# Performance work log

Hardware: AMD Instinct MI355X
Metric: run time of the kernel (lower is better)

The kernel has to match this reference:

```python
import jax, jax.numpy as jnp
import numpy as np

B, C, INTER, T, H, W = 2, 256, 64, 8, 32, 32


def setup_inputs() -> dict:
    key = jax.random.key(0)
    ks = jax.random.split(key, 4)
    scale_q = 1.0 / np.sqrt(C)
    x = jax.random.normal(ks[0], (B, C, T, H, W), dtype=jnp.float32)
    Wq = jax.random.normal(ks[1], (INTER, C), dtype=jnp.float32) * scale_q
    Wk = jax.random.normal(ks[2], (INTER, C), dtype=jnp.float32) * scale_q
    Wv = jax.random.normal(ks[3], (C, C), dtype=jnp.float32) * scale_q
    return {
        "x": x,
        "Wq": Wq, "bq": jnp.zeros((INTER,), jnp.float32),
        "Wk": Wk, "bk": jnp.zeros((INTER,), jnp.float32),
        "Wv": Wv, "bv": jnp.zeros((C,), jnp.float32),
    }


def reference(x, Wq, bq, Wk, bk, Wv, bv):
    b, c, t, h, w = x.shape
    n = t * h * w
    xf = x.reshape(b, c, n)  # [B, C, N] (row-major flatten over T,H,W)
    # 1x1x1 Conv3d == per-voxel linear projection
    q = jnp.einsum('oc,bcn->bno', Wq, xf) + bq          # [B, N, INTER]
    k = jnp.einsum('oc,bcn->bon', Wk, xf) + bk[:, None]  # [B, INTER, N]
    v = jnp.einsum('oc,bcn->bon', Wv, xf) + bv[:, None]  # [B, C, N]
    energy = jnp.einsum('bid,bdj->bij', q, k)            # [B, N, N]
    attention = jax.nn.softmax(energy, axis=-1)
    # out[b,c,i] = sum_j v[b,c,j] * attention[b,i,j]
    out = jnp.einsum('bcj,bij->bci', v, attention)       # [B, C, N]
    out = out.reshape(b, c, t, h, w) + x
    return out
```

## Files before the change

### kernel.cpp

```cpp
#include <hip/hip_runtime.h>
#include <hip/hip_bf16.h>

typedef short short8 __attribute__((ext_vector_type(8)));
typedef float float4v __attribute__((ext_vector_type(4)));

#define MFMA(a, b, c) __builtin_amdgcn_mfma_f32_16x16x32_bf16((a), (b), (c), 0, 0, 0)

typedef const __attribute__((address_space(1))) unsigned int gu32;
typedef __attribute__((address_space(3))) unsigned int lu32;
#define GLOAD_LDS16(g, l) __builtin_amdgcn_global_load_lds((gu32*)(g), (lu32*)(l), 16, 0, 0)

#define LOG2E 1.4426950408889634f

static __device__ __forceinline__ unsigned short f2bf(float f) {
    union { float f; unsigned u; } v; v.f = f;
    unsigned r = (v.u + 0x7fffu + ((v.u >> 16) & 1u)) >> 16;
    return (unsigned short)r;
}
static __device__ __forceinline__ float bf2f(unsigned short h) {
    union { unsigned u; float f; } v; v.u = ((unsigned)h) << 16;
    return v.f;
}

static __device__ __forceinline__ int qk_idx(int b, int n, int o) {
    int frag = (b * 512 + (n >> 4)) * 2 + (o >> 5);
    return frag * 512 + ((o >> 3) & 3) * 128 + (n & 15) * 8 + (o & 7);
}
static __device__ __forceinline__ int v_idx(int b, int c, int n) {
    int frag = (b * 256 + (n >> 5)) * 16 + (c >> 4);
    return frag * 512 + ((n >> 3) & 3) * 128 + (c & 15) * 8 + (n & 7);
}

__global__ void wcvt(const float* __restrict__ Wq, const float* __restrict__ Wk,
                     const float* __restrict__ Wv,
                     unsigned short* __restrict__ Whi, unsigned short* __restrict__ Wlo) {
    int idx = blockIdx.x * 256 + threadIdx.x;
    if (idx >= 384 * 256) return;
    int row = idx >> 8, c = idx & 255;
    float f;
    if (row < 64)       f = Wq[row * 256 + c];
    else if (row < 128) f = Wk[(row - 64) * 256 + c];
    else                f = Wv[(row - 128) * 256 + c];
    unsigned short hi = f2bf(f);
    Whi[idx] = hi;
    if (row < 128) Wlo[idx] = f2bf(f - bf2f(hi));
}

__global__ __launch_bounds__(256, 1) void proj(
        const float* __restrict__ x, const unsigned short* __restrict__ Whi,
        const unsigned short* __restrict__ Wlo,
        const float* __restrict__ bq, const float* __restrict__ bk,
        const float* __restrict__ bv,
        unsigned short* __restrict__ qhi_ws, unsigned short* __restrict__ qlo_ws,
        unsigned short* __restrict__ khi_ws, unsigned short* __restrict__ klo_ws,
        unsigned short* __restrict__ vws) {
    __shared__ unsigned short XThi[64 * 264];
    __shared__ unsigned short XTlo[64 * 264];

    const int tid = threadIdx.x;
    const int b  = blockIdx.x >> 7;
    const int n0 = (blockIdx.x & 127) << 6;
    const float* xb = x + b * 2097152;

    for (int p = 0; p < 16; ++p) {
        int idx = p * 256 + tid;
        int c = idx >> 4, nq = idx & 15;
        float4v xv = *reinterpret_cast<const float4v*>(xb + c * 8192 + n0 + nq * 4);
#pragma unroll
        for (int q = 0; q < 4; ++q) {
            unsigned short hi = f2bf(xv[q]);
            XThi[(nq * 4 + q) * 264 + c] = hi;
            XTlo[(nq * 4 + q) * 264 + c] = f2bf(xv[q] - bf2f(hi));
        }
    }
    __syncthreads();

    const int lane = tid & 63, w = tid >> 6;
    const int quad = lane >> 4, l16 = lane & 15;

    short8 aXhi[8], aXlo[8];
#pragma unroll
    for (int ks = 0; ks < 8; ++ks) {
        aXhi[ks] = *reinterpret_cast<const short8*>(&XThi[(w * 16 + l16) * 264 + ks * 32 + quad * 8]);
        aXlo[ks] = *reinterpret_cast<const short8*>(&XTlo[(w * 16 + l16) * 264 + ks * 32 + quad * 8]);
    }

#pragma unroll
    for (int ot = 0; ot < 8; ++ot) {
        float4v acc = {0.f, 0.f, 0.f, 0.f};
#pragma unroll
        for (int ks = 0; ks < 8; ++ks) {
            short8 bwhi = *reinterpret_cast<const short8*>(&Whi[(ot * 16 + l16) * 256 + ks * 32 + quad * 8]);
            short8 bwlo = *reinterpret_cast<const short8*>(&Wlo[(ot * 16 + l16) * 256 + ks * 32 + quad * 8]);
            acc = MFMA(aXhi[ks], bwhi, acc);
            acc = MFMA(aXlo[ks], bwhi, acc);
            acc = MFMA(aXhi[ks], bwlo, acc);
        }
        int o = ot * 16 + l16;
        float bias = (ot < 4) ? bq[o] : bk[o - 64];
#pragma unroll
        for (int r = 0; r < 4; ++r) {
            int n = n0 + w * 16 + quad * 4 + r;
            float y = acc[r] + bias;
            if (ot < 4) y *= LOG2E;
            unsigned short hi = f2bf(y);
            unsigned short lo = f2bf(y - bf2f(hi));
            if (ot < 4) {
                int id = qk_idx(b, n, o);
                qhi_ws[id] = hi; qlo_ws[id] = lo;
            } else {
                int id = qk_idx(b, n, o - 64);
                khi_ws[id] = hi; klo_ws[id] = lo;
            }
        }
    }

    float4v acc2[4][4];
#pragma unroll
    for (int mt = 0; mt < 4; ++mt)
#pragma unroll
        for (int nt = 0; nt < 4; ++nt) acc2[mt][nt] = (float4v){0.f, 0.f, 0.f, 0.f};

#pragma unroll
    for (int ks = 0; ks < 8; ++ks) {
        short8 aW[4], bX[4];
#pragma unroll
        for (int mt = 0; mt < 4; ++mt)
            aW[mt] = *reinterpret_cast<const short8*>(&Whi[(128 + w * 64 + mt * 16 + l16) * 256 + ks * 32 + quad * 8]);
#pragma unroll
        for (int nt = 0; nt < 4; ++nt)
            bX[nt] = *reinterpret_cast<const short8*>(&XThi[(nt * 16 + l16) * 264 + ks * 32 + quad * 8]);
#pragma unroll
        for (int mt = 0; mt < 4; ++mt)
#pragma unroll
            for (int nt = 0; nt < 4; ++nt)
                acc2[mt][nt] = MFMA(aW[mt], bX[nt], acc2[mt][nt]);
    }
#pragma unroll
    for (int mt = 0; mt < 4; ++mt) {
#pragma unroll
        for (int r = 0; r < 4; ++r) {
            int c = w * 64 + mt * 16 + quad * 4 + r;
            float bias = bv[c];
#pragma unroll
            for (int nt = 0; nt < 4; ++nt) {
                int n = n0 + nt * 16 + l16;
                vws[v_idx(b, c, n)] = f2bf(acc2[mt][nt][r] + bias);
            }
        }
    }
}

__global__ __launch_bounds__(512, 2) void attn(
        const unsigned short* __restrict__ qhi_ws, const unsigned short* __restrict__ qlo_ws,
        const unsigned short* __restrict__ khi_ws, const unsigned short* __restrict__ klo_ws,
        const unsigned short* __restrict__ vws,
        unsigned short* __restrict__ Opart, float* __restrict__ ml) {
    __shared__ unsigned short Vlds[3][16384];
    __shared__ unsigned short Pl[8 * 32 * 72];

    const int tid = threadIdx.x, lane = tid & 63, w = tid >> 6;
    const int quad = lane >> 4, l16 = lane & 15;
    const int xcd = blockIdx.x & 7, b = xcd & 1, jr = xcd >> 1;
    const int it = blockIdx.x >> 3;
    const int iw = it * 256 + w * 32;
    unsigned short* Pw = Pl + w * (32 * 72);

    const unsigned short* khb = khi_ws + (size_t)((b * 512 + jr * 128) * 2) * 512 + lane * 8;
    const unsigned short* klb = klo_ws + (size_t)((b * 512 + jr * 128) * 2) * 512 + lane * 8;
    const unsigned short* qhb = qhi_ws + (size_t)((b * 512 + (iw >> 4)) * 2) * 512 + lane * 8;
    const unsigned short* qlb = qlo_ws + (size_t)((b * 512 + (iw >> 4)) * 2) * 512 + lane * 8;
    const unsigned short* vstage = vws + ((size_t)(b * 256 + jr * 64) + (w >> 2)) * 8192
                                       + ((w & 3) * 4) * 512 + lane * 8;

    float4v acc[2][16];
#pragma unroll
    for (int mt = 0; mt < 2; ++mt)
#pragma unroll
        for (int cf = 0; cf < 16; ++cf) acc[mt][cf] = (float4v){0.f, 0.f, 0.f, 0.f};
    float lrow[2][4];
    short8 aP[2][2];
#pragma unroll
    for (int mt = 0; mt < 2; ++mt)
#pragma unroll
        for (int r = 0; r < 4; ++r) lrow[mt][r] = 0.f;

#pragma unroll
    for (int q = 0; q < 4; ++q)
        GLOAD_LDS16(vstage + q * 512, &Vlds[0][(w * 4 + q) * 512]);
    vstage += 16384;

    int bprev = 2, bcur = 0, bnext = 1;
#pragma unroll 1
    for (int itn = 0; itn < 32; ++itn) {
        if (itn) __syncthreads();

        if (itn < 31) {
#pragma unroll
            for (int q = 0; q < 4; ++q)
                GLOAD_LDS16(vstage + q * 512, &Vlds[bnext][(w * 4 + q) * 512]);
            vstage += 16384;
        }

        short8 qh[2][2], qlr[2][2];
#pragma unroll
        for (int mt = 0; mt < 2; ++mt)
#pragma unroll
            for (int kf = 0; kf < 2; ++kf) {
                qh[mt][kf]  = *reinterpret_cast<const short8*>(qhb + (mt * 2 + kf) * 512);
                qlr[mt][kf] = *reinterpret_cast<const short8*>(qlb + (mt * 2 + kf) * 512);
            }

        float4v s[2][4];
#pragma unroll
        for (int mt = 0; mt < 2; ++mt)
#pragma unroll
            for (int jt = 0; jt < 4; ++jt) s[mt][jt] = (float4v){0.f, 0.f, 0.f, 0.f};
#pragma unroll
        for (int jt = 0; jt < 4; ++jt) {
            short8 kh0 = *reinterpret_cast<const short8*>(khb + (jt * 2 + 0) * 512);
            short8 kh1 = *reinterpret_cast<const short8*>(khb + (jt * 2 + 1) * 512);
            short8 kl0 = *reinterpret_cast<const short8*>(klb + (jt * 2 + 0) * 512);
            short8 kl1 = *reinterpret_cast<const short8*>(klb + (jt * 2 + 1) * 512);
#pragma unroll
            for (int mt = 0; mt < 2; ++mt) {
                s[mt][jt] = MFMA(qh[mt][0],  kh0, s[mt][jt]);
                s[mt][jt] = MFMA(qlr[mt][0], kh0, s[mt][jt]);
                s[mt][jt] = MFMA(qh[mt][0],  kl0, s[mt][jt]);
                s[mt][jt] = MFMA(qh[mt][1],  kh1, s[mt][jt]);
                s[mt][jt] = MFMA(qlr[mt][1], kh1, s[mt][jt]);
                s[mt][jt] = MFMA(qh[mt][1],  kl1, s[mt][jt]);
            }
        }
        khb += 4096; klb += 4096;

        if (itn) {
            const unsigned short* vl = &Vlds[bprev][0];
#pragma unroll
            for (int cf = 0; cf < 16; ++cf) {
                short8 v0 = *reinterpret_cast<const short8*>(vl + cf * 512 + lane * 8);
                short8 v1 = *reinterpret_cast<const short8*>(vl + (16 + cf) * 512 + lane * 8);
                acc[0][cf] = MFMA(aP[0][0], v0, acc[0][cf]);
                acc[1][cf] = MFMA(aP[1][0], v0, acc[1][cf]);
                acc[0][cf] = MFMA(aP[0][1], v1, acc[0][cf]);
                acc[1][cf] = MFMA(aP[1][1], v1, acc[1][cf]);
            }
        }

#pragma unroll
        for (int mt = 0; mt < 2; ++mt)
#pragma unroll
            for (int jt = 0; jt < 4; ++jt)
#pragma unroll
                for (int r = 0; r < 4; ++r) {
                    float p_ = exp2f(s[mt][jt][r]);
                    lrow[mt][r] += p_;
                    Pw[(mt * 16 + quad * 4 + r) * 72 + jt * 16 + l16] = f2bf(p_);
                }

#pragma unroll
        for (int mt = 0; mt < 2; ++mt)
#pragma unroll
            for (int kf = 0; kf < 2; ++kf)
                aP[mt][kf] = *reinterpret_cast<const short8*>(
                    &Pw[(mt * 16 + l16) * 72 + kf * 32 + quad * 8]);

        int t = bprev; bprev = bcur; bcur = bnext; bnext = t;
    }

    {
        const unsigned short* vl = &Vlds[bprev][0];
#pragma unroll
        for (int cf = 0; cf < 16; ++cf) {
            short8 v0 = *reinterpret_cast<const short8*>(vl + cf * 512 + lane * 8);
            short8 v1 = *reinterpret_cast<const short8*>(vl + (16 + cf) * 512 + lane * 8);
            acc[0][cf] = MFMA(aP[0][0], v0, acc[0][cf]);
            acc[1][cf] = MFMA(aP[1][0], v0, acc[1][cf]);
            acc[0][cf] = MFMA(aP[0][1], v1, acc[0][cf]);
            acc[1][cf] = MFMA(aP[1][1], v1, acc[1][cf]);
        }
    }

#pragma unroll
    for (int mt = 0; mt < 2; ++mt)
#pragma unroll
        for (int r = 0; r < 4; ++r) {
            float lv = lrow[mt][r];
            lv += __shfl_xor(lv, 1);
            lv += __shfl_xor(lv, 2);
            lv += __shfl_xor(lv, 4);
            lv += __shfl_xor(lv, 8);
            if (l16 == 0) {
                int iloc = w * 32 + mt * 16 + quad * 4 + r;
                ml[blockIdx.x * 512 + iloc] = 0.0f;
                ml[blockIdx.x * 512 + 256 + iloc] = lv;
            }
        }

    unsigned short* ob = Opart + blockIdx.x * 65536;
#pragma unroll
    for (int mt = 0; mt < 2; ++mt)
#pragma unroll
        for (int cf = 0; cf < 16; ++cf)
#pragma unroll
            for (int r = 0; r < 4; ++r) {
                int iloc = w * 32 + mt * 16 + quad * 4 + r;
                ob[iloc * 256 + cf * 16 + l16] = f2bf(acc[mt][cf][r]);
            }
}

__global__ __launch_bounds__(256) void combine(
        const unsigned short* __restrict__ Opart, const float* __restrict__ ml,
        const float* __restrict__ x, float* __restrict__ out) {
    __shared__ float wfac[4][256];
    __shared__ float trans[64 * 261];

    const int t = threadIdx.x;
    const int blk = blockIdx.x;
    const int b = blk & 1, cc = (blk >> 1) & 3, it = blk >> 3;

    {
        int i = t;
        float m[4], l[4];
#pragma unroll
        for (int s = 0; s < 4; ++s) {
            int ablk = (it << 3) | (s << 1) | b;
            m[s] = ml[ablk * 512 + i];
            l[s] = ml[ablk * 512 + 256 + i];
        }
        float M = fmaxf(fmaxf(m[0], m[1]), fmaxf(m[2], m[3]));
        float wsum = 0.f, wv[4];
#pragma unroll
        for (int s = 0; s < 4; ++s) { wv[s] = exp2f(m[s] - M); wsum += wv[s] * l[s]; }
        float inv = 1.0f / wsum;
#pragma unroll
        for (int s = 0; s < 4; ++s) wfac[s][i] = wv[s] * inv;
    }
    __syncthreads();

    {
        const int c = t & 63, tr = t >> 6;
#pragma unroll 1
        for (int ip = 0; ip < 64; ++ip) {
            int i = ip * 4 + tr;
            float a = 0.f;
#pragma unroll
            for (int s = 0; s < 4; ++s) {
                int ablk = (it << 3) | (s << 1) | b;
                a += wfac[s][i] * bf2f(Opart[ablk * 65536 + i * 256 + cc * 64 + c]);
            }
            trans[c * 261 + i] = a;
        }
    }
    __syncthreads();

    {
        const int c2 = t >> 2, ti = t & 3;
        const int cg = cc * 64 + c2;
        const float* xr = x + (size_t)b * 2097152 + (size_t)cg * 8192 + it * 256;
        float* orow = out + (size_t)b * 2097152 + (size_t)cg * 8192 + it * 256;
#pragma unroll 1
        for (int k = 0; k < 16; ++k) {
            int i = ti * 4 + k * 16;
            float4v o;
#pragma unroll
            for (int r = 0; r < 4; ++r) o[r] = trans[c2 * 261 + i + r];
            float4v xv = *reinterpret_cast<const float4v*>(xr + i);
#pragma unroll
            for (int r = 0; r < 4; ++r) o[r] += xv[r];
            *reinterpret_cast<float4v*>(orow + i) = o;
        }
    }
}

extern "C" void kernel_launch(void* const* d_in, const int* in_sizes, int n_in,
                              void* d_out, int out_size, void* d_ws, size_t ws_size,
                              hipStream_t stream) {
    const float* x  = (const float*)d_in[0];
    const float* Wq = (const float*)d_in[1];
    const float* bq = (const float*)d_in[2];
    const float* Wk = (const float*)d_in[3];
    const float* bk = (const float*)d_in[4];
    const float* Wv = (const float*)d_in[5];
    const float* bv = (const float*)d_in[6];

    unsigned short* Whi = (unsigned short*)d_ws;
    unsigned short* Wlo = Whi + 384 * 256;
    unsigned short* qhi = Wlo + 128 * 256;
    unsigned short* qlo = qhi + 2 * 8192 * 64;
    unsigned short* khi = qlo + 2 * 8192 * 64;
    unsigned short* klo = khi + 2 * 8192 * 64;
    unsigned short* vws = klo + 2 * 8192 * 64;
    unsigned short* Opart = vws + 2 * 256 * 8192;
    float* ml = (float*)(Opart + 256 * 65536);

    wcvt<<<384, 256, 0, stream>>>(Wq, Wk, Wv, Whi, Wlo);
    proj<<<256, 256, 0, stream>>>(x, Whi, Wlo, bq, bk, bv, qhi, qlo, khi, klo, vws);
    attn<<<256, 512, 0, stream>>>(qhi, qlo, khi, klo, vws, Opart, ml);
    combine<<<256, 256, 0, stream>>>(Opart, ml, x, (float*)d_out);
}
```

Baseline: 265.1 us.

## Shrink attention blocks to four waves with 32-key steps and hoisted Q fragments

The attention kernel now runs 512 blocks of 256 threads instead of 256 blocks of 512. Each block covers 128 query rows, and the key loop takes 64 steps of 32 keys with a smaller V staging buffer and P tile. Q fragments are loaded once outside the loop, bf16 packing uses the hardware pair conversion, and the combine kernel is reworked for the new layout with vectorized loads of the partial outputs. The max-free softmax partials now keep only row sums, which drops the unused max term. The cost is twice as many loop iterations and barriers and more partial-output traffic, traded for more blocks in flight and lower register and LDS pressure.

```diff
diff --git a/kernel.cpp b/kernel.cpp
--- a/kernel.cpp
+++ b/kernel.cpp
@@ -20,6 +20,11 @@
 static __device__ __forceinline__ float bf2f(unsigned short h) {
     union { unsigned u; float f; } v; v.u = ((unsigned)h) << 16;
     return v.f;
+}
+static __device__ __forceinline__ unsigned pk2bf(float a, float b) {
+    union { __hip_bfloat162 h; unsigned u; } cv;
+    cv.h = __float22bfloat162_rn(make_float2(a, b));
+    return cv.u;
 }
 
 static __device__ __forceinline__ int qk_idx(int b, int n, int o) {
@@ -151,27 +156,35 @@
     }
 }
 
-__global__ __launch_bounds__(512, 2) void attn(
+__global__ __launch_bounds__(256, 2) void attn(
         const unsigned short* __restrict__ qhi_ws, const unsigned short* __restrict__ qlo_ws,
         const unsigned short* __restrict__ khi_ws, const unsigned short* __restrict__ klo_ws,
         const unsigned short* __restrict__ vws,
         unsigned short* __restrict__ Opart, float* __restrict__ ml) {
-    __shared__ unsigned short Vlds[3][16384];
-    __shared__ unsigned short Pl[8 * 32 * 72];
+    __shared__ unsigned short Vlds[3][8192];
+    __shared__ unsigned short Pl[4 * 32 * 36];
 
     const int tid = threadIdx.x, lane = tid & 63, w = tid >> 6;
     const int quad = lane >> 4, l16 = lane & 15;
     const int xcd = blockIdx.x & 7, b = xcd & 1, jr = xcd >> 1;
     const int it = blockIdx.x >> 3;
-    const int iw = it * 256 + w * 32;
-    unsigned short* Pw = Pl + w * (32 * 72);
+    const int iw16 = it * 8 + w * 2;
+    unsigned short* Pw = Pl + w * (32 * 36);
 
     const unsigned short* khb = khi_ws + (size_t)((b * 512 + jr * 128) * 2) * 512 + lane * 8;
     const unsigned short* klb = klo_ws + (size_t)((b * 512 + jr * 128) * 2) * 512 + lane * 8;
-    const unsigned short* qhb = qhi_ws + (size_t)((b * 512 + (iw >> 4)) * 2) * 512 + lane * 8;
-    const unsigned short* qlb = qlo_ws + (size_t)((b * 512 + (iw >> 4)) * 2) * 512 + lane * 8;
-    const unsigned short* vstage = vws + ((size_t)(b * 256 + jr * 64) + (w >> 2)) * 8192
-                                       + ((w & 3) * 4) * 512 + lane * 8;
+    const unsigned short* qhb = qhi_ws + (size_t)((b * 512 + iw16) * 2) * 512 + lane * 8;
+    const unsigned short* qlb = qlo_ws + (size_t)((b * 512 + iw16) * 2) * 512 + lane * 8;
+    const unsigned short* vstage = vws + ((size_t)(b * 256 + jr * 64) * 16 + w * 4) * 512 + lane * 8;
+
+    short8 qh[2][2], ql[2][2];
+#pragma unroll
+    for (int mt = 0; mt < 2; ++mt)
+#pragma unroll
+        for (int kf = 0; kf < 2; ++kf) {
+            qh[mt][kf] = *reinterpret_cast<const short8*>(qhb + (mt * 2 + kf) * 512);
+            ql[mt][kf] = *reinterpret_cast<const short8*>(qlb + (mt * 2 + kf) * 512);
+        }
 
     float4v acc[2][16];
 #pragma unroll
@@ -179,7 +192,7 @@
 #pragma unroll
         for (int cf = 0; cf < 16; ++cf) acc[mt][cf] = (float4v){0.f, 0.f, 0.f, 0.f};
     float lrow[2][4];
-    short8 aP[2][2];
+    short8 aP[2];
 #pragma unroll
     for (int mt = 0; mt < 2; ++mt)
 #pragma unroll
@@ -188,82 +201,75 @@
 #pragma unroll
     for (int q = 0; q < 4; ++q)
         GLOAD_LDS16(vstage + q * 512, &Vlds[0][(w * 4 + q) * 512]);
-    vstage += 16384;
+    vstage += 8192;
 
     int bprev = 2, bcur = 0, bnext = 1;
 #pragma unroll 1
-    for (int itn = 0; itn < 32; ++itn) {
+    for (int itn = 0; itn < 64; ++itn) {
         if (itn) __syncthreads();
 
-        if (itn < 31) {
+        if (itn < 63) {
 #pragma unroll
             for (int q = 0; q < 4; ++q)
                 GLOAD_LDS16(vstage + q * 512, &Vlds[bnext][(w * 4 + q) * 512]);
-            vstage += 16384;
-        }
-
-        short8 qh[2][2], qlr[2][2];
+            vstage += 8192;
+        }
+
+        float4v s[2][2];
 #pragma unroll
         for (int mt = 0; mt < 2; ++mt)
 #pragma unroll
-            for (int kf = 0; kf < 2; ++kf) {
-                qh[mt][kf]  = *reinterpret_cast<const short8*>(qhb + (mt * 2 + kf) * 512);
-                qlr[mt][kf] = *reinterpret_cast<const short8*>(qlb + (mt * 2 + kf) * 512);
-            }
-
-        float4v s[2][4];
-#pragma unroll
-        for (int mt = 0; mt < 2; ++mt)
-#pragma unroll
-            for (int jt = 0; jt < 4; ++jt) s[mt][jt] = (float4v){0.f, 0.f, 0.f, 0.f};
-#pragma unroll
-        for (int jt = 0; jt < 4; ++jt) {
+            for (int jt = 0; jt < 2; ++jt) s[mt][jt] = (float4v){0.f, 0.f, 0.f, 0.f};
+#pragma unroll
+        for (int jt = 0; jt < 2; ++jt) {
             short8 kh0 = *reinterpret_cast<const short8*>(khb + (jt * 2 + 0) * 512);
             short8 kh1 = *reinterpret_cast<const short8*>(khb + (jt * 2 + 1) * 512);
             short8 kl0 = *reinterpret_cast<const short8*>(klb + (jt * 2 + 0) * 512);
             short8 kl1 = *reinterpret_cast<const short8*>(klb + (jt * 2 + 1) * 512);
 #pragma unroll
             for (int mt = 0; mt < 2; ++mt) {
-                s[mt][jt] = MFMA(qh[mt][0],  kh0, s[mt][jt]);
-                s[mt][jt] = MFMA(qlr[mt][0], kh0, s[mt][jt]);
-                s[mt][jt] = MFMA(qh[mt][0],  kl0, s[mt][jt]);
-                s[mt][jt] = MFMA(qh[mt][1],  kh1, s[mt][jt]);
-                s[mt][jt] = MFMA(qlr[mt][1], kh1, s[mt][jt]);
-                s[mt][jt] = MFMA(qh[mt][1],  kl1, s[mt][jt]);
-            }
-        }
-        khb += 4096; klb += 4096;
+                s[mt][jt] = MFMA(qh[mt][0], kh0, s[mt][jt]);
+                s[mt][jt] = MFMA(ql[mt][0], kh0, s[mt][jt]);
+                s[mt][jt] = MFMA(qh[mt][0], kl0, s[mt][jt]);
+                s[mt][jt] = MFMA(qh[mt][1], kh1, s[mt][jt]);
+                s[mt][jt] = MFMA(ql[mt][1], kh1, s[mt][jt]);
+                s[mt][jt] = MFMA(qh[mt][1], kl1, s[mt][jt]);
+            }
+        }
+        khb += 2048; klb += 2048;
 
         if (itn) {
             const unsigned short* vl = &Vlds[bprev][0];
 #pragma unroll
             for (int cf = 0; cf < 16; ++cf) {
                 short8 v0 = *reinterpret_cast<const short8*>(vl + cf * 512 + lane * 8);
-                short8 v1 = *reinterpret_cast<const short8*>(vl + (16 + cf) * 512 + lane * 8);
-                acc[0][cf] = MFMA(aP[0][0], v0, acc[0][cf]);
-                acc[1][cf] = MFMA(aP[1][0], v0, acc[1][cf]);
-                acc[0][cf] = MFMA(aP[0][1], v1, acc[0][cf]);
-                acc[1][cf] = MFMA(aP[1][1], v1, acc[1][cf]);
+                acc[0][cf] = MFMA(aP[0], v0, acc[0][cf]);
+                acc[1][cf] = MFMA(aP[1], v0, acc[1][cf]);
             }
         }
 
 #pragma unroll
         for (int mt = 0; mt < 2; ++mt)
 #pragma unroll
-            for (int jt = 0; jt < 4; ++jt)
-#pragma unroll
-                for (int r = 0; r < 4; ++r) {
-                    float p_ = exp2f(s[mt][jt][r]);
-                    lrow[mt][r] += p_;
-                    Pw[(mt * 16 + quad * 4 + r) * 72 + jt * 16 + l16] = f2bf(p_);
-                }
+            for (int jt = 0; jt < 2; ++jt) {
+                float p0 = exp2f(s[mt][jt][0]);
+                float p1 = exp2f(s[mt][jt][1]);
+                float p2 = exp2f(s[mt][jt][2]);
+                float p3 = exp2f(s[mt][jt][3]);
+                lrow[mt][0] += p0; lrow[mt][1] += p1;
+                lrow[mt][2] += p2; lrow[mt][3] += p3;
+                unsigned u01 = pk2bf(p0, p1);
+                unsigned u23 = pk2bf(p2, p3);
+                int base = (mt * 16 + quad * 4) * 36 + jt * 16 + l16;
+                Pw[base]          = (unsigned short)u01;
+                Pw[base + 36]     = (unsigned short)(u01 >> 16);
+                Pw[base + 72]     = (unsigned short)u23;
+                Pw[base + 108]    = (unsigned short)(u23 >> 16);
+            }
 
 #pragma unroll
         for (int mt = 0; mt < 2; ++mt)
-#pragma unroll
-            for (int kf = 0; kf < 2; ++kf)
-                aP[mt][kf] = *reinterpret_cast<const short8*>(
-                    &Pw[(mt * 16 + l16) * 72 + kf * 32 + quad * 8]);
+            aP[mt] = *reinterpret_cast<const short8*>(&Pw[(mt * 16 + l16) * 36 + quad * 8]);
 
         int t = bprev; bprev = bcur; bcur = bnext; bnext = t;
     }
@@ -273,11 +279,8 @@
 #pragma unroll
         for (int cf = 0; cf < 16; ++cf) {
             short8 v0 = *reinterpret_cast<const short8*>(vl + cf * 512 + lane * 8);
-            short8 v1 = *reinterpret_cast<const short8*>(vl + (16 + cf) * 512 + lane * 8);
-            acc[0][cf] = MFMA(aP[0][0], v0, acc[0][cf]);
-            acc[1][cf] = MFMA(aP[1][0], v0, acc[1][cf]);
-            acc[0][cf] = MFMA(aP[0][1], v1, acc[0][cf]);
-            acc[1][cf] = MFMA(aP[1][1], v1, acc[1][cf]);
+            acc[0][cf] = MFMA(aP[0], v0, acc[0][cf]);
+            acc[1][cf] = MFMA(aP[1], v0, acc[1][cf]);
         }
     }
 
@@ -292,79 +295,78 @@
             lv += __shfl_xor(lv, 8);
             if (l16 == 0) {
                 int iloc = w * 32 + mt * 16 + quad * 4 + r;
-                ml[blockIdx.x * 512 + iloc] = 0.0f;
-                ml[blockIdx.x * 512 + 256 + iloc] = lv;
-            }
-        }
-
-    unsigned short* ob = Opart + blockIdx.x * 65536;
+                ml[blockIdx.x * 128 + iloc] = lv;
+            }
+        }
+
+    unsigned short* ob = Opart + (size_t)blockIdx.x * 32768;
 #pragma unroll
     for (int mt = 0; mt < 2; ++mt)
 #pragma unroll
-        for (int cf = 0; cf < 16; ++cf)
-#pragma unroll
-            for (int r = 0; r < 4; ++r) {
-                int iloc = w * 32 + mt * 16 + quad * 4 + r;
-                ob[iloc * 256 + cf * 16 + l16] = f2bf(acc[mt][cf][r]);
-            }
+        for (int cf = 0; cf < 16; ++cf) {
+            unsigned u01 = pk2bf(acc[mt][cf][0], acc[mt][cf][1]);
+            unsigned u23 = pk2bf(acc[mt][cf][2], acc[mt][cf][3]);
+            int iloc = w * 32 + mt * 16 + quad * 4;
+            ob[(iloc + 0) * 256 + cf * 16 + l16] = (unsigned short)u01;
+            ob[(iloc + 1) * 256 + cf * 16 + l16] = (unsigned short)(u01 >> 16);
+            ob[(iloc + 2) * 256 + cf * 16 + l16] = (unsigned short)u23;
+            ob[(iloc + 3) * 256 + cf * 16 + l16] = (unsigned short)(u23 >> 16);
+        }
 }
 
 __global__ __launch_bounds__(256) void combine(
         const unsigned short* __restrict__ Opart, const float* __restrict__ ml,
         const float* __restrict__ x, float* __restrict__ out) {
-    __shared__ float wfac[4][256];
-    __shared__ float trans[64 * 261];
+    __shared__ float fac[128];
+    __shared__ float trans[64 * 130];
 
     const int t = threadIdx.x;
     const int blk = blockIdx.x;
     const int b = blk & 1, cc = (blk >> 1) & 3, it = blk >> 3;
 
+    if (t < 128) {
+        float sum = 0.f;
+#pragma unroll
+        for (int s = 0; s < 4; ++s)
+            sum += ml[(size_t)((it << 3) | (s << 1) | b) * 128 + t];
+        fac[t] = 1.0f / sum;
+    }
+    __syncthreads();
+
     {
-        int i = t;
-        float m[4], l[4];
-#pragma unroll
-        for (int s = 0; s < 4; ++s) {
-            int ablk = (it << 3) | (s << 1) | b;
-            m[s] = ml[ablk * 512 + i];
-            l[s] = ml[ablk * 512 + 256 + i];
-        }
-        float M = fmaxf(fmaxf(m[0], m[1]), fmaxf(m[2], m[3]));
-        float wsum = 0.f, wv[4];
-#pragma unroll
-        for (int s = 0; s < 4; ++s) { wv[s] = exp2f(m[s] - M); wsum += wv[s] * l[s]; }
-        float inv = 1.0f / wsum;
-#pragma unroll
-        for (int s = 0; s < 4; ++s) wfac[s][i] = wv[s] * inv;
+        const int cgrp = t & 7, irow = t >> 3;
+#pragma unroll
+        for (int ip = 0; ip < 4; ++ip) {
+            int i = ip * 32 + irow;
+            float a[8];
+#pragma unroll
+            for (int e = 0; e < 8; ++e) a[e] = 0.f;
+#pragma unroll
+            for (int s = 0; s < 4; ++s) {
+                const unsigned short* op = Opart +
+                    (size_t)((it << 3) | (s << 1) | b) * 32768 + i * 256 + cc * 64 + cgrp * 8;
+                short8 o = *reinterpret_cast<const short8*>(op);
+#pragma unroll
+                for (int e = 0; e < 8; ++e) a[e] += bf2f((unsigned short)o[e]);
+            }
+            float f = fac[i];
+#pragma unroll
+            for (int e = 0; e < 8; ++e) trans[(cgrp * 8 + e) * 130 + i] = a[e] * f;
+        }
     }
     __syncthreads();
 
     {
-        const int c = t & 63, tr = t >> 6;
-#pragma unroll 1
-        for (int ip = 0; ip < 64; ++ip) {
-            int i = ip * 4 + tr;
-            float a = 0.f;
-#pragma unroll
-            for (int s = 0; s < 4; ++s) {
-                int ablk = (it << 3) | (s << 1) | b;
-                a += wfac[s][i] * bf2f(Opart[ablk * 65536 + i * 256 + cc * 64 + c]);
-            }
-            trans[c * 261 + i] = a;
-        }
-    }
-    __syncthreads();
-
-    {
-        const int c2 = t >> 2, ti = t & 3;
+        const int c2 = t >> 2, iq = t & 3;
         const int cg = cc * 64 + c2;
-        const float* xr = x + (size_t)b * 2097152 + (size_t)cg * 8192 + it * 256;
-        float* orow = out + (size_t)b * 2097152 + (size_t)cg * 8192 + it * 256;
-#pragma unroll 1
-        for (int k = 0; k < 16; ++k) {
-            int i = ti * 4 + k * 16;
+        const float* xr = x + (size_t)b * 2097152 + (size_t)cg * 8192 + it * 128;
+        float* orow = out + (size_t)b * 2097152 + (size_t)cg * 8192 + it * 128;
+#pragma unroll 2
+        for (int k = 0; k < 8; ++k) {
+            int i = iq * 4 + k * 16;
             float4v o;
 #pragma unroll
-            for (int r = 0; r < 4; ++r) o[r] = trans[c2 * 261 + i + r];
+            for (int r = 0; r < 4; ++r) o[r] = trans[c2 * 130 + i + r];
             float4v xv = *reinterpret_cast<const float4v*>(xr + i);
 #pragma unroll
             for (int r = 0; r < 4; ++r) o[r] += xv[r];
@@ -392,10 +394,10 @@
     unsigned short* klo = khi + 2 * 8192 * 64;
     unsigned short* vws = klo + 2 * 8192 * 64;
     unsigned short* Opart = vws + 2 * 256 * 8192;
-    float* ml = (float*)(Opart + 256 * 65536);
+    float* ml = (float*)(Opart + (size_t)512 * 32768);
 
     wcvt<<<384, 256, 0, stream>>>(Wq, Wk, Wv, Whi, Wlo);
     proj<<<256, 256, 0, stream>>>(x, Whi, Wlo, bq, bk, bv, qhi, qlo, khi, klo, vws);
-    attn<<<256, 512, 0, stream>>>(qhi, qlo, khi, klo, vws, Opart, ml);
-    combine<<<256, 256, 0, stream>>>(Opart, ml, x, (float*)d_out);
-}
+    attn<<<512, 256, 0, stream>>>(qhi, qlo, khi, klo, vws, Opart, ml);
+    combine<<<512, 256, 0, stream>>>(Opart, ml, x, (float*)d_out);
+}
```

Result: no change. 261.4 us (-1.4%).
